# Kernel tuning notes

Hardware: AMD Instinct MI355X
Metric: run time of the kernel (lower is better)

## Reference

```python
import jax, jax.numpy as jnp
import numpy as np

DIM = 1024
HEADS = 16
DHEAD = DIM // HEADS

def setup_inputs() -> dict:
    key = jax.random.key(0)
    ks = jax.random.split(key, 7)
    b, n = 4, 2048
    x = jax.random.normal(ks[0], (b, n, DIM), dtype=jnp.float32)
    bias = jax.random.normal(ks[1], (HEADS, n, n), dtype=jnp.float32) * 0.02
    w_qkv = jax.random.normal(ks[2], (DIM, 3 * DIM), dtype=jnp.float32) * (DIM ** -0.5)
    w_out = jax.random.normal(ks[3], (DIM, DIM), dtype=jnp.float32) * (DIM ** -0.5)
    b_out = jax.random.normal(ks[4], (DIM,), dtype=jnp.float32) * 0.01
    ln_gamma = jnp.ones((DIM,), dtype=jnp.float32)
    ln_beta = jnp.zeros((DIM,), dtype=jnp.float32)
    return {"x": x, "relative_position_bias": bias, "w_qkv": w_qkv,
            "w_out": w_out, "b_out": b_out, "ln_gamma": ln_gamma, "ln_beta": ln_beta}

def reference(x, relative_position_bias, w_qkv, w_out, b_out, ln_gamma, ln_beta):
    # LayerNorm
    mu = jnp.mean(x, axis=-1, keepdims=True)
    var = jnp.var(x, axis=-1, keepdims=True)
    xn = (x - mu) * jax.lax.rsqrt(var + 1e-5) * ln_gamma + ln_beta
    # QKV projection (no bias)
    qkv = xn @ w_qkv  # [b, n, 3*dim]
    q, k, v = jnp.split(qkv, 3, axis=-1)
    b, n, _ = x.shape
    def heads(t):
        return t.reshape(b, n, HEADS, DHEAD).transpose(0, 2, 1, 3)  # b h n d
    q, k, v = heads(q), heads(k), heads(v)
    scale = DHEAD ** -0.5
    scores = jnp.einsum('bhid,bhjd->bhij', q, k) * scale + relative_position_bias
    attn = jax.nn.softmax(scores, axis=-1)
    out = jnp.einsum('bhij,bhjd->bhid', attn, v)
    out = out.transpose(0, 2, 1, 3).reshape(b, n, DIM)
    return out @ w_out + b_out
```

## Files before the change

kernel.cpp:

```cpp
#include <hip/hip_runtime.h>

typedef unsigned short u16;
typedef __attribute__((ext_vector_type(8))) short s8v;
typedef __attribute__((ext_vector_type(4))) float f4v;

#define MFMA16(a, b, c) __builtin_amdgcn_mfma_f32_16x16x32_bf16((a), (b), (c), 0, 0, 0)

#define GLOAD16(gp, lp) __builtin_amdgcn_global_load_lds(                      \
    (const __attribute__((address_space(1))) void*)(gp),                       \
    (__attribute__((address_space(3))) void*)(lp), 16, 0, 0)

__device__ inline float bf2f(u16 h) { return __uint_as_float(((unsigned)h) << 16); }
__device__ inline u16 f2bf(float f) {
    unsigned u = __float_as_uint(f);
    u += 0x7FFFu + ((u >> 16) & 1u);
    return (u16)(u >> 16);
}

__global__ void probe_kernel(const u16* __restrict__ x16, int* __restrict__ flag) {
    int lane = threadIdx.x;
    int cnt = 0;
    for (int i = lane; i < 2048; i += 64) {
        float v = bf2f(x16[2 * i]);
        float a = fabsf(v);
        bool sane = (a == 0.0f) || (a > 1e-5f && a < 1e5f);
        if (!sane) cnt++;
    }
#pragma unroll
    for (int off = 32; off; off >>= 1) cnt += __shfl_xor(cnt, off);
    if (lane == 0) flag[0] = (cnt > 512) ? 1 : 0;
}

__global__ __launch_bounds__(256) void transpose_convert_kernel(
    const void* __restrict__ src, u16* __restrict__ dst,
    const int* __restrict__ flagp, int K, int N) {
    __shared__ float t[32][33];
    int f = *flagp;
    int n0 = blockIdx.x * 32, k0 = blockIdx.y * 32;
    int tid = threadIdx.x;
    int r = tid >> 3, c4 = (tid & 7) * 4;
    if (f) {
        const float* s = (const float*)src + (size_t)(k0 + r) * N + n0 + c4;
        float4 v = *(const float4*)s;
        t[r][c4] = v.x; t[r][c4 + 1] = v.y; t[r][c4 + 2] = v.z; t[r][c4 + 3] = v.w;
    } else {
        const u16* s = (const u16*)src + (size_t)(k0 + r) * N + n0 + c4;
        uint2 v = *(const uint2*)s;
        t[r][c4]     = bf2f((u16)(v.x & 0xffff));
        t[r][c4 + 1] = bf2f((u16)(v.x >> 16));
        t[r][c4 + 2] = bf2f((u16)(v.y & 0xffff));
        t[r][c4 + 3] = bf2f((u16)(v.y >> 16));
    }
    __syncthreads();
    u16 o[4];
#pragma unroll
    for (int i = 0; i < 4; i++) o[i] = f2bf(t[c4 + i][r]);
    uint2 packed;
    packed.x = (unsigned)o[0] | ((unsigned)o[1] << 16);
    packed.y = (unsigned)o[2] | ((unsigned)o[3] << 16);
    *(uint2*)(dst + (size_t)(n0 + r) * K + k0 + c4) = packed;
}

__global__ __launch_bounds__(256) void transpose_v_kernel(const u16* __restrict__ v,
                                                          u16* __restrict__ vt) {
    __shared__ u16 t[64][72];
    int bh = blockIdx.y;
    int n0 = blockIdx.x * 64;
    int tid = threadIdx.x;
    int r = tid >> 2, c = (tid & 3) * 16;
    const u16* src = v + ((size_t)bh * 2048 + n0 + r) * 64 + c;
    *(uint4*)&t[r][c]     = *(const uint4*)src;
    *(uint4*)&t[r][c + 8] = *(const uint4*)(src + 8);
    __syncthreads();
    u16 o[16];
#pragma unroll
    for (int i = 0; i < 16; i++) o[i] = t[c + i][r];
    u16* dst = vt + ((size_t)bh * 64 + r) * 2048 + n0 + c;
    *(uint4*)dst       = *(const uint4*)&o[0];
    *(uint4*)(dst + 8) = *(const uint4*)&o[8];
}

__global__ __launch_bounds__(256) void ln_kernel(const void* __restrict__ xv,
                                                 const void* __restrict__ gv,
                                                 const void* __restrict__ bv,
                                                 u16* __restrict__ xn,
                                                 const int* __restrict__ flagp) {
    int f = *flagp;
    int row = blockIdx.x;
    int tid = threadIdx.x;
    int lane = tid & 63, wave = tid >> 6;

    float v[4];
    if (f) {
        const float* xr = (const float*)xv + (size_t)row * 1024;
        float4 a = ((const float4*)xr)[tid];
        v[0] = a.x; v[1] = a.y; v[2] = a.z; v[3] = a.w;
    } else {
        const u16* xr = (const u16*)xv + (size_t)row * 1024;
        uint2 raw = ((const uint2*)xr)[tid];
        v[0] = bf2f((u16)(raw.x & 0xffff));
        v[1] = bf2f((u16)(raw.x >> 16));
        v[2] = bf2f((u16)(raw.y & 0xffff));
        v[3] = bf2f((u16)(raw.y >> 16));
    }

    float s = v[0] + v[1] + v[2] + v[3];
    float ss = v[0]*v[0] + v[1]*v[1] + v[2]*v[2] + v[3]*v[3];
#pragma unroll
    for (int off = 32; off; off >>= 1) {
        s  += __shfl_xor(s, off);
        ss += __shfl_xor(ss, off);
    }
    __shared__ float red[8];
    if (lane == 0) { red[wave] = s; red[4 + wave] = ss; }
    __syncthreads();
    s  = red[0] + red[1] + red[2] + red[3];
    ss = red[4] + red[5] + red[6] + red[7];

    float mu  = s * (1.0f / 1024.0f);
    float var = ss * (1.0f / 1024.0f) - mu * mu;
    float rs  = rsqrtf(var + 1e-5f);

    u16 o[4];
#pragma unroll
    for (int i = 0; i < 4; i++) {
        int c = tid * 4 + i;
        float g = f ? ((const float*)gv)[c] : bf2f(((const u16*)gv)[c]);
        float b = f ? ((const float*)bv)[c] : bf2f(((const u16*)bv)[c]);
        float y = (v[i] - mu) * rs * g + b;
        o[i] = f2bf(y);
    }
    uint2 packed;
    packed.x = (unsigned)o[0] | ((unsigned)o[1] << 16);
    packed.y = (unsigned)o[2] | ((unsigned)o[3] << 16);
    ((uint2*)(xn + (size_t)row * 1024))[tid] = packed;
}

template <int MODE>
__global__ __launch_bounds__(256) void gemm_kernel(const u16* __restrict__ A,
                                                   const u16* __restrict__ WT,
                                                   const void* __restrict__ bias,
                                                   const int* __restrict__ flagp,
                                                   void* __restrict__ outv,
                                                   int M, int N, int K) {
    __shared__ __align__(16) u16 As[128 * 64];
    __shared__ __align__(16) u16 Bs[128 * 64];

    int tid = threadIdx.x;
    int lane = tid & 63, wave = tid >> 6;
    int quad = lane >> 4, l16 = lane & 15;
    int wr = wave >> 1, wc = wave & 1;
    int m0 = blockIdx.y * 128, n0 = blockIdx.x * 128;

    int srow = lane >> 3;
    int sk   = (lane & 7) * 8;
    const u16* pa = A  + (size_t)(m0 + wave * 32 + srow) * K + sk;
    const u16* pb = WT + (size_t)(n0 + wave * 32 + srow) * K + sk;

    f4v acc[4][4];
#pragma unroll
    for (int i = 0; i < 4; i++)
#pragma unroll
        for (int j = 0; j < 4; j++) acc[i][j] = (f4v){0.f, 0.f, 0.f, 0.f};

    for (int k0 = 0; k0 < K; k0 += 64) {
        __syncthreads();
#pragma unroll
        for (int cs = 0; cs < 4; cs++) {
            GLOAD16(pa + (size_t)cs * 8 * K + k0, &As[(wave * 32 + cs * 8) * 64]);
            GLOAD16(pb + (size_t)cs * 8 * K + k0, &Bs[(wave * 32 + cs * 8) * 64]);
        }
        __syncthreads();

#pragma unroll
        for (int kc = 0; kc < 2; kc++) {
            s8v afr[4], bfr[4];
#pragma unroll
            for (int mi = 0; mi < 4; mi++)
                afr[mi] = *(const s8v*)&As[(wr * 64 + mi * 16 + l16) * 64 + kc * 32 + quad * 8];
#pragma unroll
            for (int ni = 0; ni < 4; ni++)
                bfr[ni] = *(const s8v*)&Bs[(wc * 64 + ni * 16 + l16) * 64 + kc * 32 + quad * 8];
#pragma unroll
            for (int mi = 0; mi < 4; mi++)
#pragma unroll
                for (int ni = 0; ni < 4; ni++)
                    acc[mi][ni] = MFMA16(afr[mi], bfr[ni], acc[mi][ni]);
        }
    }

    int f = (MODE == 1) ? *flagp : 0;

#pragma unroll
    for (int mi = 0; mi < 4; mi++) {
#pragma unroll
        for (int ni = 0; ni < 4; ni++) {
#pragma unroll
            for (int r = 0; r < 4; r++) {
                int gm = m0 + wr * 64 + mi * 16 + quad * 4 + r;
                int gn = n0 + wc * 64 + ni * 16 + l16;
                float v = acc[mi][ni][r];
                if (MODE == 1) {
                    float bb = f ? ((const float*)bias)[gn]
                                 : bf2f(((const u16*)bias)[gn]);
                    ((float*)outv)[(size_t)gm * N + gn] = v + bb;
                } else {
                    u16* out = (u16*)outv;
                    int sel = gn >> 10, rem = gn & 1023;
                    int h = rem >> 6, d = rem & 63;
                    int b = gm >> 11, q = gm & 2047;
                    size_t dst = ((size_t)(b * 16 + h) * 2048 + q) * 64 + d;
                    out[(size_t)sel * 8388608 + dst] = f2bf(v);
                }
            }
        }
    }
}

__global__ __launch_bounds__(256) void attn_kernel(const u16* __restrict__ qg,
                                                   const u16* __restrict__ kg,
                                                   const u16* __restrict__ vtg,
                                                   const void* __restrict__ bias,
                                                   const int* __restrict__ flagp,
                                                   u16* __restrict__ out) {
    int d_ = blockIdx.x;
    int xcd = d_ & 7, t_ = d_ >> 3;
    int b = t_ & 3;
    int g = (t_ >> 2) * 8 + xcd;
    int h = g & 15, qt = g >> 4;
    int q0 = qt * 64;
    int bh = b * 16 + h;
    int f = *flagp;

    int tid = threadIdx.x;
    int lane = tid & 63, wave = tid >> 6;
    int quad = lane >> 4, l16 = lane & 15;

    __shared__ __align__(16) u16 Ks[64 * 64];
    __shared__ __align__(16) u16 Vt[64 * 64];
    __shared__ __align__(16) u16 Ps[4][16][72];

    const u16* qrow = qg + ((size_t)bh * 2048 + q0 + wave * 16 + l16) * 64;
    s8v qf0 = *(const s8v*)(qrow + quad * 8);
    s8v qf1 = *(const s8v*)(qrow + 32 + quad * 8);

    f4v oacc[4];
#pragma unroll
    for (int i = 0; i < 4; i++) oacc[i] = (f4v){0.f, 0.f, 0.f, 0.f};
    float mrow[4] = {-1e30f, -1e30f, -1e30f, -1e30f};
    float lrow[4] = {0.f, 0.f, 0.f, 0.f};

    const u16* kbase = kg + (size_t)bh * 2048 * 64;
    const u16* vbase = vtg + (size_t)bh * 64 * 2048;

    int srow = lane >> 3;
    int scol = ((lane & 7) ^ srow) * 16;
    const char* kp = (const char*)kbase + ((size_t)(wave * 16 + srow)) * 128 + scol;
    const char* vp = (const char*)vbase + ((size_t)(wave * 16 + srow)) * 4096 + scol;
    u16* ksl = &Ks[wave * 16 * 64];
    u16* vsl = &Vt[wave * 16 * 64];

    int xr = (l16 & 7) << 4;

    size_t boff = ((size_t)h * 2048 + q0 + wave * 16 + quad * 4) * 2048;
    const float* bbf = (const float*)bias + boff;
    const u16*   bbh = (const u16*)bias + boff;

    for (int kt = 0; kt < 2048; kt += 64) {
        __syncthreads();
        GLOAD16(kp, ksl);
        GLOAD16(kp + 1024, ksl + 512);
        GLOAD16(vp, vsl);
        GLOAD16(vp + 8 * 4096, vsl + 512);
        kp += 64 * 128;
        vp += 128;
        __syncthreads();

        f4v sc[4];
#pragma unroll
        for (int ni = 0; ni < 4; ni++) {
            const char* krow = (const char*)Ks + (ni * 16 + l16) * 128;
            s8v k0f = *(const s8v*)(krow + ((quad * 16) ^ xr));
            s8v k1f = *(const s8v*)(krow + ((64 + quad * 16) ^ xr));
            f4v t = (f4v){0.f, 0.f, 0.f, 0.f};
            t = MFMA16(qf0, k0f, t);
            t = MFMA16(qf1, k1f, t);
            sc[ni] = t;
        }

        float barr[4][4];
        if (f) {
#pragma unroll
            for (int r = 0; r < 4; r++)
#pragma unroll
                for (int ni = 0; ni < 4; ni++)
                    barr[ni][r] = bbf[(size_t)r * 2048 + kt + ni * 16 + l16];
        } else {
#pragma unroll
            for (int r = 0; r < 4; r++)
#pragma unroll
                for (int ni = 0; ni < 4; ni++)
                    barr[ni][r] = bf2f(bbh[(size_t)r * 2048 + kt + ni * 16 + l16]);
        }
        float sv[4][4];
#pragma unroll
        for (int r = 0; r < 4; r++)
#pragma unroll
            for (int ni = 0; ni < 4; ni++)
                sv[ni][r] = sc[ni][r] * 0.125f + barr[ni][r];

        float mx[4];
#pragma unroll
        for (int r = 0; r < 4; r++) {
            mx[r] = fmaxf(fmaxf(sv[0][r], sv[1][r]), fmaxf(sv[2][r], sv[3][r]));
#pragma unroll
            for (int off = 1; off < 16; off <<= 1)
                mx[r] = fmaxf(mx[r], __shfl_xor(mx[r], off));
        }
        float alpha[4], rsum[4];
#pragma unroll
        for (int r = 0; r < 4; r++) {
            float mnew = fmaxf(mrow[r], mx[r]);
            alpha[r] = __expf(mrow[r] - mnew);
            mrow[r] = mnew;
            rsum[r] = 0.f;
#pragma unroll
            for (int ni = 0; ni < 4; ni++) {
                float p = __expf(sv[ni][r] - mnew);
                rsum[r] += p;
                Ps[wave][quad * 4 + r][ni * 16 + l16] = f2bf(p);
            }
        }
#pragma unroll
        for (int r = 0; r < 4; r++) {
#pragma unroll
            for (int off = 1; off < 16; off <<= 1)
                rsum[r] += __shfl_xor(rsum[r], off);
            lrow[r] = lrow[r] * alpha[r] + rsum[r];
        }
#pragma unroll
        for (int od = 0; od < 4; od++) {
            f4v t = oacc[od];
            t[0] *= alpha[0]; t[1] *= alpha[1]; t[2] *= alpha[2]; t[3] *= alpha[3];
            oacc[od] = t;
        }

        s8v pf0 = *(const s8v*)&Ps[wave][l16][quad * 8];
        s8v pf1 = *(const s8v*)&Ps[wave][l16][32 + quad * 8];
#pragma unroll
        for (int od = 0; od < 4; od++) {
            const char* vrow = (const char*)Vt + (od * 16 + l16) * 128;
            s8v vf0 = *(const s8v*)(vrow + ((quad * 16) ^ xr));
            s8v vf1 = *(const s8v*)(vrow + ((64 + quad * 16) ^ xr));
            oacc[od] = MFMA16(pf0, vf0, oacc[od]);
            oacc[od] = MFMA16(pf1, vf1, oacc[od]);
        }
    }

    float inv[4];
#pragma unroll
    for (int r = 0; r < 4; r++) inv[r] = 1.0f / lrow[r];
#pragma unroll
    for (int od = 0; od < 4; od++) {
#pragma unroll
        for (int r = 0; r < 4; r++) {
            size_t dst = ((size_t)b * 2048 + q0 + wave * 16 + quad * 4 + r) * 1024 +
                         h * 64 + od * 16 + l16;
            out[dst] = f2bf(oacc[od][r] * inv[r]);
        }
    }
}

extern "C" void kernel_launch(void* const* d_in, const int* in_sizes, int n_in,
                              void* d_out, int out_size, void* d_ws, size_t ws_size,
                              hipStream_t stream) {
    const void* x      = d_in[0];
    const void* bias   = d_in[1];
    const void* w_qkv  = d_in[2];
    const void* w_out  = d_in[3];
    const void* b_out  = d_in[4];
    const void* gamma  = d_in[5];
    const void* beta   = d_in[6];

    u16* base = (u16*)d_ws;
    int* flag = (int*)d_ws;
    u16* xn   = base + 64;
    u16* qkv  = xn + 8388608;
    u16* attn = qkv + 3 * 8388608;
    u16* wqT  = attn + 8388608;
    u16* woT  = wqT + 3145728;

    probe_kernel<<<dim3(1), dim3(64), 0, stream>>>((const u16*)x, flag);

    ln_kernel<<<dim3(8192), dim3(256), 0, stream>>>(x, gamma, beta, xn, flag);

    transpose_convert_kernel<<<dim3(96, 32), dim3(256), 0, stream>>>(
        w_qkv, wqT, flag, 1024, 3072);
    transpose_convert_kernel<<<dim3(32, 32), dim3(256), 0, stream>>>(
        w_out, woT, flag, 1024, 1024);

    gemm_kernel<0><<<dim3(3072 / 128, 8192 / 128), dim3(256), 0, stream>>>(
        xn, wqT, nullptr, flag, qkv, 8192, 3072, 1024);

    transpose_v_kernel<<<dim3(32, 64), dim3(256), 0, stream>>>(
        qkv + 2 * 8388608, xn);

    attn_kernel<<<dim3(2048), dim3(256), 0, stream>>>(
        qkv, qkv + 8388608, xn, bias, flag, attn);

    gemm_kernel<1><<<dim3(1024 / 128, 8192 / 128), dim3(256), 0, stream>>>(
        attn, woT, b_out, flag, d_out, 8192, 1024, 1024);
}
```

Measured before the change: 719.8 us.

## Double-buffer GEMM, remap blocks per XCD, and stream K/V directly in attention

```diff
diff --git a/kernel.cpp b/kernel.cpp
--- a/kernel.cpp
+++ b/kernel.cpp
@@ -143,14 +143,20 @@
                                                    const int* __restrict__ flagp,
                                                    void* __restrict__ outv,
                                                    int M, int N, int K) {
-    __shared__ __align__(16) u16 As[128 * 64];
-    __shared__ __align__(16) u16 Bs[128 * 64];
+    __shared__ __align__(16) u16 As[2][128 * 64];
+    __shared__ __align__(16) u16 Bs[2][128 * 64];
 
     int tid = threadIdx.x;
     int lane = tid & 63, wave = tid >> 6;
     int quad = lane >> 4, l16 = lane & 15;
     int wr = wave >> 1, wc = wave & 1;
-    int m0 = blockIdx.y * 128, n0 = blockIdx.x * 128;
+
+    int nx = N >> 7, ny = M >> 7;
+    int nb = nx * ny, cpx = nb >> 3;
+    int bid = blockIdx.x;
+    int l = (bid & 7) * cpx + (bid >> 3);
+    int by = l / nx, bx = l - by * nx;
+    int m0 = by * 128, n0 = bx * 128;
 
     int srow = lane >> 3;
     int sk   = (lane & 7) * 8;
@@ -163,30 +169,45 @@
 #pragma unroll
         for (int j = 0; j < 4; j++) acc[i][j] = (f4v){0.f, 0.f, 0.f, 0.f};
 
-    for (int k0 = 0; k0 < K; k0 += 64) {
-        __syncthreads();
-#pragma unroll
-        for (int cs = 0; cs < 4; cs++) {
-            GLOAD16(pa + (size_t)cs * 8 * K + k0, &As[(wave * 32 + cs * 8) * 64]);
-            GLOAD16(pb + (size_t)cs * 8 * K + k0, &Bs[(wave * 32 + cs * 8) * 64]);
-        }
-        __syncthreads();
-
+    const int NT = K >> 6;
+#pragma unroll
+    for (int cs = 0; cs < 4; cs++) {
+        GLOAD16(pa + (size_t)cs * 8 * K, &As[0][(wave * 32 + cs * 8) * 64]);
+        GLOAD16(pb + (size_t)cs * 8 * K, &Bs[0][(wave * 32 + cs * 8) * 64]);
+    }
+    __syncthreads();
+
+    int cur = 0;
+    for (int t = 0; t < NT; ++t) {
+        if (t + 1 < NT) {
+            int k0 = (t + 1) << 6;
+#pragma unroll
+            for (int cs = 0; cs < 4; cs++) {
+                GLOAD16(pa + (size_t)cs * 8 * K + k0, &As[cur ^ 1][(wave * 32 + cs * 8) * 64]);
+                GLOAD16(pb + (size_t)cs * 8 * K + k0, &Bs[cur ^ 1][(wave * 32 + cs * 8) * 64]);
+            }
+        }
+        const u16* Ac = &As[cur][0];
+        const u16* Bc = &Bs[cur][0];
 #pragma unroll
         for (int kc = 0; kc < 2; kc++) {
             s8v afr[4], bfr[4];
 #pragma unroll
             for (int mi = 0; mi < 4; mi++)
-                afr[mi] = *(const s8v*)&As[(wr * 64 + mi * 16 + l16) * 64 + kc * 32 + quad * 8];
+                afr[mi] = *(const s8v*)&Ac[(wr * 64 + mi * 16 + l16) * 64 + kc * 32 + quad * 8];
 #pragma unroll
             for (int ni = 0; ni < 4; ni++)
-                bfr[ni] = *(const s8v*)&Bs[(wc * 64 + ni * 16 + l16) * 64 + kc * 32 + quad * 8];
+                bfr[ni] = *(const s8v*)&Bc[(wc * 64 + ni * 16 + l16) * 64 + kc * 32 + quad * 8];
+            __builtin_amdgcn_s_setprio(1);
 #pragma unroll
             for (int mi = 0; mi < 4; mi++)
 #pragma unroll
                 for (int ni = 0; ni < 4; ni++)
                     acc[mi][ni] = MFMA16(afr[mi], bfr[ni], acc[mi][ni]);
-        }
+            __builtin_amdgcn_s_setprio(0);
+        }
+        __syncthreads();
+        cur ^= 1;
     }
 
     int f = (MODE == 1) ? *flagp : 0;
@@ -236,8 +257,6 @@
     int lane = tid & 63, wave = tid >> 6;
     int quad = lane >> 4, l16 = lane & 15;
 
-    __shared__ __align__(16) u16 Ks[64 * 64];
-    __shared__ __align__(16) u16 Vt[64 * 64];
     __shared__ __align__(16) u16 Ps[4][16][72];
 
     const u16* qrow = qg + ((size_t)bh * 2048 + q0 + wave * 16 + l16) * 64;
@@ -253,40 +272,24 @@
     const u16* kbase = kg + (size_t)bh * 2048 * 64;
     const u16* vbase = vtg + (size_t)bh * 64 * 2048;
 
-    int srow = lane >> 3;
-    int scol = ((lane & 7) ^ srow) * 16;
-    const char* kp = (const char*)kbase + ((size_t)(wave * 16 + srow)) * 128 + scol;
-    const char* vp = (const char*)vbase + ((size_t)(wave * 16 + srow)) * 4096 + scol;
-    u16* ksl = &Ks[wave * 16 * 64];
-    u16* vsl = &Vt[wave * 16 * 64];
-
-    int xr = (l16 & 7) << 4;
-
     size_t boff = ((size_t)h * 2048 + q0 + wave * 16 + quad * 4) * 2048;
     const float* bbf = (const float*)bias + boff;
     const u16*   bbh = (const u16*)bias + boff;
 
     for (int kt = 0; kt < 2048; kt += 64) {
-        __syncthreads();
-        GLOAD16(kp, ksl);
-        GLOAD16(kp + 1024, ksl + 512);
-        GLOAD16(vp, vsl);
-        GLOAD16(vp + 8 * 4096, vsl + 512);
-        kp += 64 * 128;
-        vp += 128;
-        __syncthreads();
-
         f4v sc[4];
+        __builtin_amdgcn_s_setprio(1);
 #pragma unroll
         for (int ni = 0; ni < 4; ni++) {
-            const char* krow = (const char*)Ks + (ni * 16 + l16) * 128;
-            s8v k0f = *(const s8v*)(krow + ((quad * 16) ^ xr));
-            s8v k1f = *(const s8v*)(krow + ((64 + quad * 16) ^ xr));
+            const u16* kr = kbase + (size_t)(kt + ni * 16 + l16) * 64 + quad * 8;
+            s8v k0f = *(const s8v*)kr;
+            s8v k1f = *(const s8v*)(kr + 32);
             f4v t = (f4v){0.f, 0.f, 0.f, 0.f};
             t = MFMA16(qf0, k0f, t);
             t = MFMA16(qf1, k1f, t);
             sc[ni] = t;
         }
+        __builtin_amdgcn_s_setprio(0);
 
         float barr[4][4];
         if (f) {
@@ -317,16 +320,31 @@
             for (int off = 1; off < 16; off <<= 1)
                 mx[r] = fmaxf(mx[r], __shfl_xor(mx[r], off));
         }
-        float alpha[4], rsum[4];
+        bool need = (mx[0] > mrow[0] + 8.f) || (mx[1] > mrow[1] + 8.f) ||
+                    (mx[2] > mrow[2] + 8.f) || (mx[3] > mrow[3] + 8.f);
+        if (__any(need)) {
+            float al[4];
+#pragma unroll
+            for (int r = 0; r < 4; r++) {
+                float mnew = fmaxf(mrow[r], mx[r]);
+                al[r] = __expf(mrow[r] - mnew);
+                mrow[r] = mnew;
+                lrow[r] *= al[r];
+            }
+#pragma unroll
+            for (int od = 0; od < 4; od++) {
+                f4v t = oacc[od];
+                t[0] *= al[0]; t[1] *= al[1]; t[2] *= al[2]; t[3] *= al[3];
+                oacc[od] = t;
+            }
+        }
+        float rsum[4];
 #pragma unroll
         for (int r = 0; r < 4; r++) {
-            float mnew = fmaxf(mrow[r], mx[r]);
-            alpha[r] = __expf(mrow[r] - mnew);
-            mrow[r] = mnew;
             rsum[r] = 0.f;
 #pragma unroll
             for (int ni = 0; ni < 4; ni++) {
-                float p = __expf(sv[ni][r] - mnew);
+                float p = __expf(sv[ni][r] - mrow[r]);
                 rsum[r] += p;
                 Ps[wave][quad * 4 + r][ni * 16 + l16] = f2bf(p);
             }
@@ -336,25 +354,21 @@
 #pragma unroll
             for (int off = 1; off < 16; off <<= 1)
                 rsum[r] += __shfl_xor(rsum[r], off);
-            lrow[r] = lrow[r] * alpha[r] + rsum[r];
-        }
-#pragma unroll
-        for (int od = 0; od < 4; od++) {
-            f4v t = oacc[od];
-            t[0] *= alpha[0]; t[1] *= alpha[1]; t[2] *= alpha[2]; t[3] *= alpha[3];
-            oacc[od] = t;
+            lrow[r] += rsum[r];
         }
 
         s8v pf0 = *(const s8v*)&Ps[wave][l16][quad * 8];
         s8v pf1 = *(const s8v*)&Ps[wave][l16][32 + quad * 8];
+        __builtin_amdgcn_s_setprio(1);
 #pragma unroll
         for (int od = 0; od < 4; od++) {
-            const char* vrow = (const char*)Vt + (od * 16 + l16) * 128;
-            s8v vf0 = *(const s8v*)(vrow + ((quad * 16) ^ xr));
-            s8v vf1 = *(const s8v*)(vrow + ((64 + quad * 16) ^ xr));
+            const u16* vr = vbase + (size_t)(od * 16 + l16) * 2048 + kt + quad * 8;
+            s8v vf0 = *(const s8v*)vr;
+            s8v vf1 = *(const s8v*)(vr + 32);
             oacc[od] = MFMA16(pf0, vf0, oacc[od]);
             oacc[od] = MFMA16(pf1, vf1, oacc[od]);
         }
+        __builtin_amdgcn_s_setprio(0);
     }
 
     float inv[4];
@@ -399,7 +413,7 @@
     transpose_convert_kernel<<<dim3(32, 32), dim3(256), 0, stream>>>(
         w_out, woT, flag, 1024, 1024);
 
-    gemm_kernel<0><<<dim3(3072 / 128, 8192 / 128), dim3(256), 0, stream>>>(
+    gemm_kernel<0><<<dim3(1536), dim3(256), 0, stream>>>(
         xn, wqT, nullptr, flag, qkv, 8192, 3072, 1024);
 
     transpose_v_kernel<<<dim3(32, 64), dim3(256), 0, stream>>>(
@@ -408,6 +422,6 @@
     attn_kernel<<<dim3(2048), dim3(256), 0, stream>>>(
         qkv, qkv + 8388608, xn, bias, flag, attn);
 
-    gemm_kernel<1><<<dim3(1024 / 128, 8192 / 128), dim3(256), 0, stream>>>(
+    gemm_kernel<1><<<dim3(512), dim3(256), 0, stream>>>(
         attn, woT, b_out, flag, d_out, 8192, 1024, 1024);
 }
```

Measured after the change: 987.6 us. 37.2% more time.
